# Kernel tuning notes

Measured on AMD Instinct MI355X. Metric: run time of the kernel, lower is better.

The kernel has to match this reference:

```python
import jax, jax.numpy as jnp
import numpy as np


def setup_inputs() -> dict:
    key = jax.random.key(0)
    k0, k1, k2, k3, k4 = jax.random.split(key, 5)
    B, W, C, C2, D = 4, 64, 512, 512, 64  # D = C // k, k=8
    x = jax.random.normal(k0, (B, W, W, C), dtype=jnp.float32)
    input_h = jax.random.normal(k1, (B, W, W, C2), dtype=jnp.float32)
    f = jax.random.normal(k2, (1, 1, C2, D), dtype=jnp.float32) * 0.02
    g = jax.random.normal(k3, (1, 1, C, D), dtype=jnp.float32) * 0.02
    gamma = jax.random.uniform(k4, (1,), dtype=jnp.float32)
    return {"x": x, "input_h": input_h, "f": f, "g": g, "gamma": gamma}


def reference(x, input_h, f, g, gamma):
    # x: [B,W,W,C] NHWC, input_h: [B,W,W,C2], f: [1,1,C2,D], g: [1,1,C,D]
    B, W, _, C = x.shape
    C2 = input_h.shape[-1]
    N = W * W
    # 1x1 convs == per-pixel channel matmuls
    f_proj = jnp.einsum('bhwc,cd->bhwd', input_h, f[0, 0])  # [B,W,W,D]
    g_proj = jnp.einsum('bhwc,cd->bhwd', x, g[0, 0])        # [B,W,W,D]
    f_flat = f_proj.reshape(B, N, -1)
    g_flat = g_proj.reshape(B, N, -1)
    # unscaled attention scores over spatial positions
    s = jnp.einsum('bnd,bmd->bnm', g_flat, f_flat)          # [B,N,N]
    beta = jax.nn.softmax(s, axis=-1)
    h_flat = input_h.reshape(B, N, C2)
    o = jnp.einsum('bnm,bmc->bnc', beta, h_flat).reshape(B, W, W, C2)
    # mix_concat == 'mix': learned residual mix
    return gamma * o + x
```

## Files before the change

kernel.cpp:

```cpp
#include <hip/hip_runtime.h>
#include <hip/hip_bf16.h>
#include <cstdint>
#include <cstddef>


#define NPOS 4096
#define CCH  512
#define DQK  64
#define LSTR 72

typedef __attribute__((ext_vector_type(8)))  short s8v;
typedef __attribute__((ext_vector_type(4)))  short s4v;
typedef __attribute__((ext_vector_type(4)))  float f4v;

__device__ __forceinline__ float bf2f(unsigned short u) {
    unsigned int x = ((unsigned int)u) << 16;
    return __builtin_bit_cast(float, x);
}
__device__ __forceinline__ unsigned short f2bf(float f) {
    unsigned int u = __builtin_bit_cast(unsigned int, f);
    u += 0x7fffu + ((u >> 16) & 1u);
    return (unsigned short)(u >> 16);
}

__global__ __launch_bounds__(256) void wt_kernel(
    const float* __restrict__ f, const float* __restrict__ g,
    unsigned short* __restrict__ fT, unsigned short* __restrict__ gT)
{
    int gid = blockIdx.x * 256 + threadIdx.x;
    for (int e = 0; e < 4; ++e) {
        int i = e * 16384 + gid;
        int which = i >> 15;
        int j = i & 32767;
        int d = j >> 9, k = j & 511;
        const float* s = which ? g : f;
        unsigned short* dst = which ? gT : fT;
        dst[j] = f2bf(s[k * 64 + d]);
    }
}

__global__ __launch_bounds__(256) void proj_kernel(
    const float* __restrict__ x,  const float* __restrict__ ih,
    const unsigned short* __restrict__ gT, const unsigned short* __restrict__ fT,
    unsigned short* __restrict__ Qg, unsigned short* __restrict__ Kf)
{
    __shared__ __align__(16) short Alds[128 * LSTR];
    __shared__ __align__(16) short Wlds[64 * LSTR];
    const int tid = threadIdx.x;
    const int wave = tid >> 6, lane = tid & 63;
    const int n15 = lane & 15, quad = lane >> 4;
    const int which = blockIdx.x >> 7;
    const int rb = (blockIdx.x & 127) * 128;
    const float* src = which ? ih : x;
    const unsigned short* wT  = which ? fT : gT;
    unsigned short* dst = which ? Kf : Qg;

    f4v acc[2][4];
    for (int i = 0; i < 2; ++i)
        for (int j = 0; j < 4; ++j)
            acc[i][j] = f4v{0.f, 0.f, 0.f, 0.f};

    for (int kc = 0; kc < 8; ++kc) {
        for (int p = 0; p < 8; ++p) {
            int idx = p * 256 + tid;
            int r = idx >> 4, gg = idx & 15;
            f4v v = *(const f4v*)(src + (size_t)(rb + r) * CCH + kc * 64 + gg * 4);
            s4v tv;
            for (int j = 0; j < 4; ++j) tv[j] = (short)f2bf(v[j]);
            *(s4v*)&Alds[r * LSTR + gg * 4] = tv;
        }
        for (int p = 0; p < 2; ++p) {
            int idx = p * 256 + tid;
            int c = idx >> 3, gg = idx & 7;
            *(s8v*)&Wlds[c * LSTR + gg * 8] =
                *(const s8v*)(wT + (size_t)c * CCH + kc * 64 + gg * 8);
        }
        __syncthreads();
        for (int kk = 0; kk < 2; ++kk) {
            s8v af0 = *(const s8v*)&Alds[(wave * 32 +      n15) * LSTR + kk * 32 + quad * 8];
            s8v af1 = *(const s8v*)&Alds[(wave * 32 + 16 + n15) * LSTR + kk * 32 + quad * 8];
            for (int ct = 0; ct < 4; ++ct) {
                s8v bf = *(const s8v*)&Wlds[(ct * 16 + n15) * LSTR + kk * 32 + quad * 8];
                acc[0][ct] = __builtin_amdgcn_mfma_f32_16x16x32_bf16(af0, bf, acc[0][ct], 0, 0, 0);
                acc[1][ct] = __builtin_amdgcn_mfma_f32_16x16x32_bf16(af1, bf, acc[1][ct], 0, 0, 0);
            }
        }
        __syncthreads();
    }
    for (int rt = 0; rt < 2; ++rt)
        for (int ct = 0; ct < 4; ++ct)
            for (int r = 0; r < 4; ++r) {
                int row = wave * 32 + rt * 16 + quad * 4 + r;
                int col = ct * 16 + n15;
                dst[(size_t)(rb + row) * DQK + col] = f2bf(acc[rt][ct][r]);
            }
}

__global__ __launch_bounds__(512) void flash_kernel(
    const unsigned short* __restrict__ Qg,
    const unsigned short* __restrict__ Kf,
    const float* __restrict__ ihv,
    const float* __restrict__ xin,
    const float* __restrict__ gptr,
    float* __restrict__ out)
{
    __shared__ __align__(16) short Klds[2 * 64 * LSTR];
    __shared__ __align__(16) short Plds[64 * LSTR];
    __shared__ float l_s[64];

    const int tid = threadIdx.x;
    const int wave = tid >> 6;
    const int lane = tid & 63;
    const int n15 = lane & 15, quad = lane >> 4;
    const int bid = blockIdx.x;
    const int xcd = bid & 7;
    const int b = xcd >> 1;
    const int qt = (xcd & 1) + ((bid >> 3) << 1);
    const int qbase = qt * 64;

    const float SOFT_M = 20.0f;
    float lpart = 0.0f;

    f4v acc[4][4];
    for (int i = 0; i < 4; ++i)
        for (int j = 0; j < 4; ++j)
            acc[i][j] = f4v{0.f, 0.f, 0.f, 0.f};

    const int ti = wave >> 1;
    const int mi0 = (wave & 1) * 2;
    s8v qf[2];
    {
        const unsigned short* qp =
            Qg + ((size_t)b * NPOS + qbase + ti * 16 + n15) * DQK + quad * 8;
        qf[0] = *(const s8v*)(qp);
        qf[1] = *(const s8v*)(qp + 32);
    }

    const float* Vb = ihv + (size_t)b * NPOS * CCH;
    const int cb = wave * 64;

    const int kr = tid >> 3, kg = tid & 7;
    const unsigned short* kbase_p = Kf + ((size_t)b * NPOS + kr) * DQK + kg * 8;
    s8v kreg = *(const s8v*)(kbase_p);

    for (int kb = 0; kb < NPOS / 64; ++kb) {
        const int m0 = kb * 64;
        *(s8v*)&Klds[(kb & 1) * 64 * LSTR + kr * LSTR + kg * 8] = kreg;
        if (kb + 1 < NPOS / 64)
            kreg = *(const s8v*)(kbase_p + (size_t)(m0 + 64) * DQK);
        s8v vf[4][2];
        for (int ct = 0; ct < 4; ++ct) {
            const float* vp = Vb + (size_t)(m0 + quad * 8) * CCH + cb + ct * 16 + n15;
            for (int kk = 0; kk < 2; ++kk) {
                s8v t;
                for (int j = 0; j < 8; ++j)
                    t[j] = (short)f2bf(vp[(size_t)(kk * 32 + j) * CCH]);
                vf[ct][kk] = t;
            }
        }
        __syncthreads();

        {
            const short* Kb = &Klds[(kb & 1) * 64 * LSTR];
            for (int mm = 0; mm < 2; ++mm) {
                const int mi = mi0 + mm;
                f4v s4 = f4v{0.f, 0.f, 0.f, 0.f};
                for (int ks = 0; ks < 2; ++ks) {
                    s8v kf = *(const s8v*)&Kb[(mi * 16 + n15) * LSTR + ks * 32 + quad * 8];
                    s4 = __builtin_amdgcn_mfma_f32_16x16x32_bf16(qf[ks], kf, s4, 0, 0, 0);
                }
                const int col = mi * 16 + n15;
                const int row0 = ti * 16 + quad * 4;
                for (int r = 0; r < 4; ++r)
                    Plds[(row0 + r) * LSTR + col] =
                        (short)f2bf(__expf(fminf(s4[r], 80.0f) - SOFT_M));
            }
        }
        __syncthreads();

        {
            const int r = tid >> 3, j8 = tid & 7;
            s8v p8 = *(const s8v*)&Plds[r * LSTR + j8 * 8];
            float ls = 0.f;
            for (int e = 0; e < 8; ++e) ls += bf2f((unsigned short)p8[e]);
            lpart += ls;
        }
        for (int kk = 0; kk < 2; ++kk) {
            s8v af[4];
            for (int q4 = 0; q4 < 4; ++q4)
                af[q4] = *(const s8v*)&Plds[(q4 * 16 + n15) * LSTR + kk * 32 + quad * 8];
            for (int q4 = 0; q4 < 4; ++q4)
                for (int ct = 0; ct < 4; ++ct)
                    acc[q4][ct] = __builtin_amdgcn_mfma_f32_16x16x32_bf16(
                        af[q4], vf[ct][kk], acc[q4][ct], 0, 0, 0);
        }
    }

    lpart += __shfl_xor(lpart, 1);
    lpart += __shfl_xor(lpart, 2);
    lpart += __shfl_xor(lpart, 4);
    if ((tid & 7) == 0) l_s[tid >> 3] = lpart;
    __syncthreads();

    const float gamma = gptr[0];
    for (int q4 = 0; q4 < 4; ++q4) {
        for (int r = 0; r < 4; ++r) {
            const int row = q4 * 16 + quad * 4 + r;
            const float sc = gamma / l_s[row];
            for (int ct = 0; ct < 4; ++ct) {
                const int col = cb + ct * 16 + n15;
                const size_t idx = ((size_t)b * NPOS + qbase + row) * CCH + col;
                out[idx] = acc[q4][ct][r] * sc + xin[idx];
            }
        }
    }
}

extern "C" void kernel_launch(void* const* d_in, const int* in_sizes, int n_in,
                              void* d_out, int out_size, void* d_ws, size_t ws_size,
                              hipStream_t stream)
{
    const float* x     = (const float*)d_in[0];
    const float* ih    = (const float*)d_in[1];
    const float* f     = (const float*)d_in[2];
    const float* g     = (const float*)d_in[3];
    const float* gamma = (const float*)d_in[4];
    float* out = (float*)d_out;

    char* ws = (char*)d_ws;
    unsigned short* fT = (unsigned short*)(ws + 0);
    unsigned short* gT = (unsigned short*)(ws + 65536);
    unsigned short* Qg = (unsigned short*)(ws + 131072);
    unsigned short* Kf = (unsigned short*)(ws + 2228224);

    wt_kernel<<<64, 256, 0, stream>>>(f, g, fT, gT);
    proj_kernel<<<256, 256, 0, stream>>>(x, ih, gT, fT, Qg, Kf);
    flash_kernel<<<256, 512, 0, stream>>>(Qg, Kf, ih, x, gamma, out);
}
```

Measured before the change: 297.0 us.

## Pre-transpose V to bf16 channel-major layout for vectorized flash loads

Adds a kernel that converts input_h to bf16 and transposes it to [B, C, N] in workspace. The flash kernel then loads V fragments as two 16-byte vector reads per tile instead of sixteen strided fp32 scalar loads with per-element conversion. This cuts the global traffic and instruction count in the inner loop. The cost is an extra kernel launch and a full pass over input_h, which adds about 16 MB of writes and reads.

Result: faster. 279.5 us (-5.9%).

```diff
diff --git a/kernel.cpp b/kernel.cpp
--- a/kernel.cpp
+++ b/kernel.cpp
@@ -36,6 +36,33 @@
         const float* s = which ? g : f;
         unsigned short* dst = which ? gT : fT;
         dst[j] = f2bf(s[k * 64 + d]);
+    }
+}
+
+__global__ __launch_bounds__(256) void vt_kernel(
+    const float* __restrict__ ih, unsigned short* __restrict__ Vt)
+{
+    __shared__ unsigned short T[64 * 65];
+    const int tid = threadIdx.x;
+    const int bidx = blockIdx.x;
+    const int bb = bidx >> 9;
+    const int rem = bidx & 511;
+    const int ct = rem >> 6;
+    const int nt = rem & 63;
+
+    for (int p = 0; p < 4; ++p) {
+        int idx = p * 256 + tid;
+        int r = idx >> 4, gg = idx & 15;
+        f4v v = *(const f4v*)(ih + ((size_t)bb * NPOS + nt * 64 + r) * CCH + ct * 64 + gg * 4);
+        for (int j = 0; j < 4; ++j) T[r * 65 + gg * 4 + j] = f2bf(v[j]);
+    }
+    __syncthreads();
+    for (int p = 0; p < 2; ++p) {
+        int idx = p * 256 + tid;
+        int c = idx >> 3, ng = idx & 7;
+        unsigned short tmp[8];
+        for (int j = 0; j < 8; ++j) tmp[j] = T[(ng * 8 + j) * 65 + c];
+        *(s8v*)(Vt + ((size_t)bb * CCH + ct * 64 + c) * NPOS + nt * 64 + ng * 8) = *(const s8v*)tmp;
     }
 }
 
@@ -99,7 +126,7 @@
 __global__ __launch_bounds__(512) void flash_kernel(
     const unsigned short* __restrict__ Qg,
     const unsigned short* __restrict__ Kf,
-    const float* __restrict__ ihv,
+    const unsigned short* __restrict__ Vt,
     const float* __restrict__ xin,
     const float* __restrict__ gptr,
     float* __restrict__ out)
@@ -136,8 +163,8 @@
         qf[1] = *(const s8v*)(qp + 32);
     }
 
-    const float* Vb = ihv + (size_t)b * NPOS * CCH;
     const int cb = wave * 64;
+    const unsigned short* Vb = Vt + (size_t)b * CCH * NPOS;
 
     const int kr = tid >> 3, kg = tid & 7;
     const unsigned short* kbase_p = Kf + ((size_t)b * NPOS + kr) * DQK + kg * 8;
@@ -150,13 +177,10 @@
             kreg = *(const s8v*)(kbase_p + (size_t)(m0 + 64) * DQK);
         s8v vf[4][2];
         for (int ct = 0; ct < 4; ++ct) {
-            const float* vp = Vb + (size_t)(m0 + quad * 8) * CCH + cb + ct * 16 + n15;
-            for (int kk = 0; kk < 2; ++kk) {
-                s8v t;
-                for (int j = 0; j < 8; ++j)
-                    t[j] = (short)f2bf(vp[(size_t)(kk * 32 + j) * CCH]);
-                vf[ct][kk] = t;
-            }
+            const unsigned short* vp =
+                Vb + (size_t)(cb + ct * 16 + n15) * NPOS + m0 + quad * 8;
+            vf[ct][0] = *(const s8v*)(vp);
+            vf[ct][1] = *(const s8v*)(vp + 32);
         }
         __syncthreads();
 
@@ -232,8 +256,10 @@
     unsigned short* gT = (unsigned short*)(ws + 65536);
     unsigned short* Qg = (unsigned short*)(ws + 131072);
     unsigned short* Kf = (unsigned short*)(ws + 2228224);
+    unsigned short* Vt = (unsigned short*)(ws + 4325376);
 
     wt_kernel<<<64, 256, 0, stream>>>(f, g, fT, gT);
+    vt_kernel<<<2048, 256, 0, stream>>>(ih, Vt);
     proj_kernel<<<256, 256, 0, stream>>>(x, ih, gT, fT, Qg, Kf);
-    flash_kernel<<<256, 512, 0, stream>>>(Qg, Kf, ih, x, gamma, out);
-}
+    flash_kernel<<<256, 512, 0, stream>>>(Qg, Kf, Vt, x, gamma, out);
+}
```
